# Kernel tuning notes

Hardware: AMD Instinct MI355X
Metric: run time of the kernel (lower is better)

## Reference

```python
import jax, jax.numpy as jnp
import numpy as np

B, T, C, H = 2, 1024, 768, 12
D = C // H
HID = 4 * C
EPS_YAT = 1e-6
EPS_LN = 1e-6


def yat_dense(x, kernel, bias, alpha):
    # scale = (sqrt(n_out)/log(1+n_out))**alpha
    y = x @ kernel
    dist = (jnp.sum(x * x, axis=-1, keepdims=True)
            + jnp.sum(kernel * kernel, axis=0) - 2.0 * y)
    y = (y * y) / (dist + EPS_YAT)
    if bias is not None:
        y = y + bias
    n = kernel.shape[1]
    scale = (jnp.sqrt(jnp.float32(n)) / jnp.log1p(jnp.float32(n))) ** alpha
    return y * scale


def layernorm(x, scale):
    mu = jnp.mean(x, axis=-1, keepdims=True)
    var = jnp.mean((x - mu) ** 2, axis=-1, keepdims=True)
    return (x - mu) * jax.lax.rsqrt(var + EPS_LN) * scale


def rope_table(seq_len, dim):
    freqs = jnp.exp(jnp.arange(0, dim, 2, dtype=jnp.float32)
                    * (-jnp.log(10000.0) / dim))
    angles = jnp.arange(seq_len, dtype=jnp.float32)[:, None] * freqs[None, :]
    return jnp.concatenate([jnp.cos(angles), jnp.sin(angles)], axis=-1)  # [T, D]


def block_forward(x, mask, p):
    Bc, Tc, Cc = x.shape
    h = layernorm(x, p['ln1_scale'])
    qkv = yat_dense(h, p['w_qkv'], p['b_qkv'], p['a_qkv'])  # [B,T,3C]
    qkv = qkv.reshape(Bc, Tc, 3, H, D)
    q, k, v = qkv[:, :, 0], qkv[:, :, 1], qkv[:, :, 2]      # [B,T,H,D]
    rope = rope_table(Tc, D)[:, None, :]                     # [T,1,D]
    q = q * rope
    k = k * rope
    scale = 1.0 / jnp.sqrt(jnp.float32(D))
    attn = jnp.einsum('bihd,bjhd->bhij', q, k) * scale       # [B,H,T,T]
    attn = jnp.where(mask, attn, jnp.finfo(attn.dtype).min)
    attn = jax.nn.softmax(attn, axis=-1)
    o = jnp.einsum('bhij,bjhd->bihd', attn, v).reshape(Bc, Tc, Cc)
    o = yat_dense(o, p['w_ao'], p['b_ao'], p['a_ao'])
    x = x + o
    h = layernorm(x, p['ln2_scale'])
    gate = yat_dense(h, p['w_fc'], p['b_fc'], p['a_fc'])
    u = yat_dense(h, p['w_gate'], p['b_gate'], p['a_gate'])
    u = jax.nn.gelu(u) * gate
    u = yat_dense(u, p['w_proj'], p['b_proj'], p['a_proj'])
    return x + u


def setup_inputs() -> dict:
    key = jax.random.key(0)
    ks = jax.random.split(key, 8)
    x = jax.random.normal(ks[0], (B, T, C), dtype=jnp.float32)
    mask = jnp.tril(jnp.ones((T, T), dtype=bool))[None, None]  # causal [1,1,T,T]
    w = lambda k, shp: 0.02 * jax.random.normal(k, shp, dtype=jnp.float32)
    return {
        'x': x, 'mask': mask,
        'ln1_scale': jnp.ones((C,), jnp.float32),
        'w_qkv': w(ks[1], (C, 3 * C)), 'b_qkv': jnp.zeros((3 * C,), jnp.float32),
        'a_qkv': jnp.ones((1,), jnp.float32),
        'w_ao': w(ks[2], (C, C)), 'b_ao': jnp.zeros((C,), jnp.float32),
        'a_ao': jnp.ones((1,), jnp.float32),
        'ln2_scale': jnp.ones((C,), jnp.float32),
        'w_fc': w(ks[3], (C, HID)), 'b_fc': jnp.zeros((HID,), jnp.float32),
        'a_fc': jnp.ones((1,), jnp.float32),
        'w_gate': w(ks[4], (C, HID)), 'b_gate': jnp.zeros((HID,), jnp.float32),
        'a_gate': jnp.ones((1,), jnp.float32),
        'w_proj': w(ks[5], (HID, C)), 'b_proj': jnp.zeros((C,), jnp.float32),
        'a_proj': jnp.ones((1,), jnp.float32),
    }


def reference(x, mask, ln1_scale, w_qkv, b_qkv, a_qkv, w_ao, b_ao, a_ao,
              ln2_scale, w_fc, b_fc, a_fc, w_gate, b_gate, a_gate,
              w_proj, b_proj, a_proj):
    p = dict(ln1_scale=ln1_scale, w_qkv=w_qkv, b_qkv=b_qkv, a_qkv=a_qkv,
             w_ao=w_ao, b_ao=b_ao, a_ao=a_ao, ln2_scale=ln2_scale,
             w_fc=w_fc, b_fc=b_fc, a_fc=a_fc, w_gate=w_gate, b_gate=b_gate,
             a_gate=a_gate, w_proj=w_proj, b_proj=b_proj, a_proj=a_proj)
    return block_forward(x, mask, p)
```

## Files before the change

kernel.cpp:

```cpp
#include <hip/hip_runtime.h>
#include <cstdint>

#define DEVFN static __device__ __forceinline__

typedef __bf16 bf16x8 __attribute__((ext_vector_type(8)));
typedef float f32x4 __attribute__((ext_vector_type(4)));
typedef unsigned short us4 __attribute__((ext_vector_type(4)));

DEVFN unsigned short f2bf(float f) {
  unsigned u = __float_as_uint(f);
  u += 0x7fffu + ((u >> 16) & 1u);
  return (unsigned short)(u >> 16);
}
DEVFN float bf2f(unsigned short h) { return __uint_as_float(((unsigned)h) << 16); }
DEVFN void async16(const void* g, void* l) {
  __builtin_amdgcn_global_load_lds((__attribute__((address_space(1))) const void*)g,
                                   (__attribute__((address_space(3))) void*)l, 16, 0, 0);
}
DEVFN float gelu_t(float u) {
  return 0.5f * u * (1.f + tanhf(0.7978845608028654f * (u + 0.044715f * u * u * u)));
}
DEVFN int xcd_swizzle(int lin, int total) {
  return (lin & 7) * (total >> 3) + (lin >> 3);
}

struct PrepArgs {
  float* rope;
  const float* W[5]; unsigned short* Wt[5]; float* cn[5];
  int N[5]; int off[6];
  const float* x; const float* g1s; unsigned short* h1; float* hrow1;
};
__global__ __launch_bounds__(256) void k_prep(PrepArgs a) {
  __shared__ float tile[32][33];
  __shared__ float part[8][32];
  __shared__ float red[12];
  const int bid = blockIdx.x, tid = threadIdx.x;
  if (bid < 256) {
    int g = bid * 256 + tid;
    int t = g >> 6, dd = g & 63, i = dd & 31;
    float fr = __expf(-0.2878231366242558f * (float)i);
    float ang = (float)t * fr;
    a.rope[g] = (dd < 32) ? cosf(ang) : sinf(ang);
  } else if (bid < 9472) {
    int lin = bid - 256;
    int e = 0;
    while (lin >= a.off[e + 1]) ++e;
    int local = lin - a.off[e];
    const int N = a.N[e];
    int nbx = N >> 5;
    int tn = local % nbx, tk = local / nbx;
    const float* W = a.W[e];
    unsigned short* Wt = a.Wt[e];
    float* cn = a.cn[e];
    const int K = (e == 4) ? 3072 : 768;
    int tx = tid & 31, ty = tid >> 5;
    float acc = 0.f;
    #pragma unroll
    for (int j = 0; j < 4; ++j) {
      int r = ty + j * 8;
      float v = W[(long)(tk * 32 + r) * N + tn * 32 + tx];
      tile[r][tx] = v;
      acc += v * v;
    }
    part[ty][tx] = acc;
    __syncthreads();
    #pragma unroll
    for (int j = 0; j < 4; ++j) {
      int rr = ty + j * 8;
      Wt[(long)(tn * 32 + rr) * K + tk * 32 + tx] = f2bf(tile[tx][rr]);
    }
    if (ty == 0) {
      float s = part[0][tx];
      #pragma unroll
      for (int jj = 1; jj < 8; ++jj) s += part[jj][tx];
      atomicAdd(&cn[tn * 32 + tx], s);
    }
  } else {
    int row = bid - 9472;
    const float* xr = a.x + (long)row * 768;
    float v0 = xr[tid], v1 = xr[tid + 256], v2 = xr[tid + 512];
    float s = v0 + v1 + v2;
    float ss = v0 * v0 + v1 * v1 + v2 * v2;
    #pragma unroll
    for (int o = 32; o; o >>= 1) { s += __shfl_xor(s, o); ss += __shfl_xor(ss, o); }
    int wv = tid >> 6;
    if ((tid & 63) == 0) { red[wv] = s; red[wv + 4] = ss; }
    __syncthreads();
    s = red[0] + red[1] + red[2] + red[3];
    ss = red[4] + red[5] + red[6] + red[7];
    float mu = s * (1.f / 768.f);
    float var = ss * (1.f / 768.f) - mu * mu;
    float rs = rsqrtf(var + 1e-6f);
    float h0 = (v0 - mu) * rs * a.g1s[tid];
    float h1 = (v1 - mu) * rs * a.g1s[tid + 256];
    float h2 = (v2 - mu) * rs * a.g1s[tid + 512];
    unsigned short* hr = a.h1 + (long)row * 768;
    hr[tid] = f2bf(h0); hr[tid + 256] = f2bf(h1); hr[tid + 512] = f2bf(h2);
    float p = h0 * h0 + h1 * h1 + h2 * h2;
    #pragma unroll
    for (int o = 32; o; o >>= 1) p += __shfl_xor(p, o);
    if ((tid & 63) == 0) red[8 + wv] = p;
    __syncthreads();
    if (tid == 0) a.hrow1[row] = red[8] + red[9] + red[10] + red[11];
  }
}

__global__ __launch_bounds__(256) void k_ln(const float* __restrict__ x,
    const float* __restrict__ g, unsigned short* __restrict__ h, float* __restrict__ row2) {
  int row = blockIdx.x, tid = threadIdx.x;
  const float* xr = x + (long)row * 768;
  float v0 = xr[tid], v1 = xr[tid + 256], v2 = xr[tid + 512];
  float s = v0 + v1 + v2;
  float ss = v0 * v0 + v1 * v1 + v2 * v2;
  #pragma unroll
  for (int o = 32; o; o >>= 1) { s += __shfl_xor(s, o); ss += __shfl_xor(ss, o); }
  __shared__ float red[12];
  int wv = tid >> 6;
  if ((tid & 63) == 0) { red[wv] = s; red[wv + 4] = ss; }
  __syncthreads();
  s = red[0] + red[1] + red[2] + red[3];
  ss = red[4] + red[5] + red[6] + red[7];
  float mu = s * (1.f / 768.f);
  float var = ss * (1.f / 768.f) - mu * mu;
  float rs = rsqrtf(var + 1e-6f);
  float h0 = (v0 - mu) * rs * g[tid];
  float h1 = (v1 - mu) * rs * g[tid + 256];
  float h2 = (v2 - mu) * rs * g[tid + 512];
  unsigned short* hr = h + (long)row * 768;
  hr[tid] = f2bf(h0); hr[tid + 256] = f2bf(h1); hr[tid + 512] = f2bf(h2);
  float p = h0 * h0 + h1 * h1 + h2 * h2;
  #pragma unroll
  for (int o = 32; o; o >>= 1) p += __shfl_xor(p, o);
  if ((tid & 63) == 0) red[8 + wv] = p;
  __syncthreads();
  if (tid == 0) row2[row] = red[8] + red[9] + red[10] + red[11];
}

constexpr int M_QKV = 0, M_AO = 1, M_PART = 2;

struct GemmArgs {
  const unsigned short* A; const unsigned short* Bt;
  const float* arow2; const float* wcol2; const float* bias; const float* alpha;
  int N; int ks;
  const float* rope;
  unsigned short* qo; unsigned short* ko; unsigned short* vo;
  const float* xf; float* xo;
  float* part;
};

template <int MODE, int NI, int NBM, int NBN, int NZ>
__global__ __launch_bounds__(256, 4) void k_gemm(GemmArgs p) {
  __shared__ __align__(16) unsigned short As[3][2048];
  __shared__ __align__(16) unsigned short Bs[3][4096];
  const int tid = threadIdx.x, wave = tid >> 6, lane = tid & 63;
  const int quad = lane >> 4, l = lane & 15;
  constexpr int TOTAL = NBM * NBN * NZ;
  const int g = xcd_swizzle(blockIdx.x, TOTAL);
  const int bm = (g % NBM) * 64;
  const int rest = g / NBM;
  const int bn = (rest % NBN) * 128;
  const int z = rest / NBN;
  const int kb = z * (NI * 32);
  const int ks = p.ks;
  const int wm = (wave & 1) * 32, wn = (wave >> 1) * 64;
  const f32x4 fzero = {0.f, 0.f, 0.f, 0.f};
  f32x4 acc[2][4];
  #pragma unroll
  for (int i = 0; i < 2; ++i)
    #pragma unroll
    for (int j = 0; j < 4; ++j) acc[i][j] = fzero;
  const int sw = (l >> 1) & 3;

  auto stage = [&](int s, int k0) {
    {
      int ci = tid;
      int r = ci >> 2;
      int c = (ci & 3) ^ ((r >> 1) & 3);
      async16(p.A + (long)(bm + r) * ks + kb + k0 + c * 8, &As[s][ci * 8]);
    }
    #pragma unroll
    for (int it = 0; it < 2; ++it) {
      int ci = tid + it * 256;
      int r = ci >> 2;
      int c = (ci & 3) ^ ((r >> 1) & 3);
      async16(p.Bt + (long)(bn + r) * ks + kb + k0 + c * 8, &Bs[s][ci * 8]);
    }
  };
  auto compute = [&](int s) {
    bf16x8 af[2], bfv[4];
    #pragma unroll
    for (int mi = 0; mi < 2; ++mi)
      af[mi] = *(const bf16x8*)&As[s][(wm + mi * 16 + l) * 32 + ((quad ^ sw) * 8)];
    #pragma unroll
    for (int ni = 0; ni < 4; ++ni)
      bfv[ni] = *(const bf16x8*)&Bs[s][(wn + ni * 16 + l) * 32 + ((quad ^ sw) * 8)];
    #pragma unroll
    for (int mi = 0; mi < 2; ++mi)
      #pragma unroll
      for (int ni = 0; ni < 4; ++ni)
        acc[mi][ni] = __builtin_amdgcn_mfma_f32_16x16x32_bf16(af[mi], bfv[ni], acc[mi][ni], 0, 0, 0);
  };
  auto iter = [&](int s, int i) {
    if (i + 1 >= NI) { asm volatile("s_waitcnt vmcnt(0)" ::: "memory"); }
    else             { asm volatile("s_waitcnt vmcnt(3)" ::: "memory"); }
    __builtin_amdgcn_s_barrier();
    asm volatile("" ::: "memory");
    if (i + 2 < NI) stage(s == 0 ? 2 : s - 1, (i + 2) * 32);
    compute(s);
  };

  stage(0, 0);
  stage(1, 32);
  int i = 0;
  while (i < NI) {
    iter(0, i); ++i;
    iter(1, i); ++i;
    iter(2, i); ++i;
  }

  if constexpr (MODE == M_PART) {
    float* slab = p.part + (long)z * (2048 * 768);
    #pragma unroll
    for (int ni = 0; ni < 4; ++ni) {
      const int j = bn + wn + ni * 16 + l;
      #pragma unroll
      for (int mi = 0; mi < 2; ++mi) {
        const int i0 = bm + wm + mi * 16 + quad * 4;
        #pragma unroll
        for (int rg = 0; rg < 4; ++rg)
          slab[(long)(i0 + rg) * 768 + j] = acc[mi][ni][rg];
      }
    }
  } else {
    const float al = p.alpha[0];
    const float nn = (float)p.N;
    const float ys = powf(sqrtf(nn) / log1pf(nn), al);
    #pragma unroll
    for (int ni = 0; ni < 4; ++ni) {
      const int j = bn + wn + ni * 16 + l;
      const float w2 = p.wcol2[j];
      const float bj = p.bias[j];
      int s3 = 0, hh = 0, dd = 0;
      if constexpr (MODE == M_QKV) { s3 = j / 768; int rem = j - s3 * 768; hh = rem >> 6; dd = rem & 63; }
      #pragma unroll
      for (int mi = 0; mi < 2; ++mi) {
        const int i0 = bm + wm + mi * 16 + quad * 4;
        float vv[4];
        #pragma unroll
        for (int rg = 0; rg < 4; ++rg) {
          const float y = acc[mi][ni][rg];
          const float dist = p.arow2[i0 + rg] + w2 - 2.f * y + 1e-6f;
          vv[rg] = (y * y / dist + bj) * ys;
        }
        if constexpr (MODE == M_QKV) {
          int b = i0 >> 10, t0 = i0 & 1023;
          if (s3 == 2) {
            us4 pk = {f2bf(vv[0]), f2bf(vv[1]), f2bf(vv[2]), f2bf(vv[3])};
            *(us4*)&p.vo[((long)(b * 12 + hh) * 64 + dd) * 1024 + t0] = pk;
          } else {
            unsigned short* dst = (s3 == 0) ? p.qo : p.ko;
            #pragma unroll
            for (int rg = 0; rg < 4; ++rg) {
              float ro = p.rope[(t0 + rg) * 64 + dd];
              dst[((long)(b * 12 + hh) * 1024 + t0 + rg) * 64 + dd] = f2bf(vv[rg] * ro);
            }
          }
        } else {
          #pragma unroll
          for (int rg = 0; rg < 4; ++rg) {
            long idx = (long)(i0 + rg) * 768 + j;
            p.xo[idx] = p.xf[idx] + vv[rg];
          }
        }
      }
    }
  }
}

struct EpiArgs {
  const float* slab; const float* arow2; const float* wcol2;
  const float* bias; const float* alpha; const float* xo; float* outf;
};
__global__ __launch_bounds__(256) void k_proj_epi(EpiArgs p) {
  int g = blockIdx.x * 256 + threadIdx.x;
  int i = g / 192, jv = (g - i * 192) * 4;
  long base = (long)i * 768 + jv;
  f32x4 y = *(const f32x4*)(p.slab + base);
  y += *(const f32x4*)(p.slab + 1572864 + base);
  const float a2 = p.arow2[i];
  const float ys = powf(sqrtf(768.f) / log1pf(768.f), p.alpha[0]);
  f32x4 xo4 = *(const f32x4*)(p.xo + base);
  f32x4 out;
  #pragma unroll
  for (int c = 0; c < 4; ++c) {
    float yy = y[c];
    float dist = a2 + p.wcol2[jv + c] - 2.f * yy + 1e-6f;
    out[c] = xo4[c] + (yy * yy / dist + p.bias[jv + c]) * ys;
  }
  *(f32x4*)(p.outf + base) = out;
}

struct MlpArgs {
  const unsigned short* A; const unsigned short* Bf; const unsigned short* Bg;
  const float* arow2; const float* w2f; const float* w2g;
  const float* bf; const float* bg; const float* af_; const float* ag_;
  unsigned short* mlp; float* mrow2;
};

__global__ __launch_bounds__(256, 2) void k_mlp(MlpArgs p) {
  constexpr int NI = 24, K = 768;
  __shared__ __align__(16) unsigned short As[3][4096];
  __shared__ __align__(16) unsigned short Bfs[3][4096];
  __shared__ __align__(16) unsigned short Bgs[3][4096];
  const int tid = threadIdx.x, wave = tid >> 6, lane = tid & 63;
  const int quad = lane >> 4, l = lane & 15;
  const int g = xcd_swizzle(blockIdx.x, 16 * 24);
  const int bm = (g % 16) * 128, bn = (g / 16) * 128;
  const int wm = (wave & 1) * 64, wn = (wave >> 1) * 64;
  const f32x4 fzero = {0.f, 0.f, 0.f, 0.f};
  f32x4 accf[4][4], accg[4][4];
  #pragma unroll
  for (int i = 0; i < 4; ++i)
    #pragma unroll
    for (int j = 0; j < 4; ++j) { accf[i][j] = fzero; accg[i][j] = fzero; }
  const int sw = (l >> 1) & 3;

  auto stage = [&](int s, int k0) {
    #pragma unroll
    for (int it = 0; it < 2; ++it) {
      int ci = tid + it * 256;
      int r = ci >> 2;
      int c = (ci & 3) ^ ((r >> 1) & 3);
      async16(p.A  + (long)(bm + r) * K + k0 + c * 8, &As[s][ci * 8]);
      async16(p.Bf + (long)(bn + r) * K + k0 + c * 8, &Bfs[s][ci * 8]);
      async16(p.Bg + (long)(bn + r) * K + k0 + c * 8, &Bgs[s][ci * 8]);
    }
  };
  auto compute = [&](int s) {
    bf16x8 af[4], bff[4], bfg[4];
    #pragma unroll
    for (int mi = 0; mi < 4; ++mi)
      af[mi] = *(const bf16x8*)&As[s][(wm + mi * 16 + l) * 32 + ((quad ^ sw) * 8)];
    #pragma unroll
    for (int ni = 0; ni < 4; ++ni) {
      bff[ni] = *(const bf16x8*)&Bfs[s][(wn + ni * 16 + l) * 32 + ((quad ^ sw) * 8)];
      bfg[ni] = *(const bf16x8*)&Bgs[s][(wn + ni * 16 + l) * 32 + ((quad ^ sw) * 8)];
    }
    #pragma unroll
    for (int mi = 0; mi < 4; ++mi)
      #pragma unroll
      for (int ni = 0; ni < 4; ++ni) {
        accf[mi][ni] = __builtin_amdgcn_mfma_f32_16x16x32_bf16(af[mi], bff[ni], accf[mi][ni], 0, 0, 0);
        accg[mi][ni] = __builtin_amdgcn_mfma_f32_16x16x32_bf16(af[mi], bfg[ni], accg[mi][ni], 0, 0, 0);
      }
  };
  auto iter = [&](int s, int i) {
    if (i + 1 >= NI) { asm volatile("s_waitcnt vmcnt(0)" ::: "memory"); }
    else             { asm volatile("s_waitcnt vmcnt(6)" ::: "memory"); }
    __builtin_amdgcn_s_barrier();
    asm volatile("" ::: "memory");
    if (i + 2 < NI) stage(s == 0 ? 2 : s - 1, (i + 2) * 32);
    compute(s);
  };

  stage(0, 0);
  stage(1, 32);
  int i = 0;
  while (i < NI) {
    iter(0, i); ++i;
    iter(1, i); ++i;
    iter(2, i); ++i;
  }

  const float ysf = powf(sqrtf(3072.f) / log1pf(3072.f), p.af_[0]);
  const float ysg = powf(sqrtf(3072.f) / log1pf(3072.f), p.ag_[0]);
  float w2f[4], w2g[4], bjf[4], bjg[4]; int js[4];
  #pragma unroll
  for (int ni = 0; ni < 4; ++ni) {
    int j = bn + wn + ni * 16 + l;
    js[ni] = j; w2f[ni] = p.w2f[j]; w2g[ni] = p.w2g[j]; bjf[ni] = p.bf[j]; bjg[ni] = p.bg[j];
  }
  #pragma unroll
  for (int mi = 0; mi < 4; ++mi) {
    #pragma unroll
    for (int rg = 0; rg < 4; ++rg) {
      const int ii = bm + wm + mi * 16 + quad * 4 + rg;
      const float a2 = p.arow2[ii];
      float rsum = 0.f;
      #pragma unroll
      for (int ni = 0; ni < 4; ++ni) {
        float yf = accf[mi][ni][rg];
        float gate = (yf * yf / (a2 + w2f[ni] - 2.f * yf + 1e-6f) + bjf[ni]) * ysf;
        float yg = accg[mi][ni][rg];
        float u  = (yg * yg / (a2 + w2g[ni] - 2.f * yg + 1e-6f) + bjg[ni]) * ysg;
        float out = gelu_t(u) * gate;
        p.mlp[(long)ii * 3072 + js[ni]] = f2bf(out);
        rsum += out * out;
      }
      #pragma unroll
      for (int o = 8; o; o >>= 1) rsum += __shfl_xor(rsum, o);
      if (l == 0) atomicAdd(&p.mrow2[ii], rsum);
    }
  }
}

__global__ __launch_bounds__(256) void k_attn(const unsigned short* __restrict__ qb,
    const unsigned short* __restrict__ kb, const unsigned short* __restrict__ vb,
    unsigned short* __restrict__ ob, float* __restrict__ orow2) {
  __shared__ __align__(16) unsigned short Qs[4096];
  __shared__ __align__(16) unsigned short Ks[3][4096];
  __shared__ __align__(16) unsigned short Vs[3][4096];
  __shared__ __align__(16) unsigned short Ps[4096];
  const int tid = threadIdx.x, wave = tid >> 6, lane = tid & 63;
  const int quad = lane >> 4, l = lane & 15;
  const int g = xcd_swizzle(blockIdx.x, 16 * 24);
  const int bh = g % 24, qt = 15 - (g / 24);
  const int b = bh / 12, hh = bh % 12;
  const int q0 = qt * 64;
  const f32x4 fzero = {0.f, 0.f, 0.f, 0.f};

  auto stage_kv = [&](int s, int jt) {
    const unsigned short* kg = kb + ((long)bh * 1024 + jt * 64) * 64;
    const unsigned short* vg = vb + (long)bh * 64 * 1024 + jt * 64;
    #pragma unroll
    for (int it = 0; it < 2; ++it) {
      int ci = tid + it * 256;
      int r = ci >> 3;
      int c = (ci & 7) ^ (r & 7);
      async16(kg + (long)r * 64 + c * 8, &Ks[s][ci * 8]);
      async16(vg + (long)r * 1024 + c * 8, &Vs[s][ci * 8]);
    }
  };

  const unsigned short* qg = qb + ((long)bh * 1024 + q0) * 64;
  #pragma unroll
  for (int it = 0; it < 2; ++it) {
    int ci = tid + it * 256;
    int r = ci >> 3;
    int c = (ci & 7) ^ (r & 7);
    async16(qg + (long)r * 64 + c * 8, &Qs[ci * 8]);
  }
  stage_kv(0, 0);
  if (qt >= 1) {
    stage_kv(1, 1);
    asm volatile("s_waitcnt vmcnt(4)" ::: "memory");
  } else {
    asm volatile("s_waitcnt vmcnt(0)" ::: "memory");
  }
  __builtin_amdgcn_s_barrier();
  asm volatile("" ::: "memory");

  bf16x8 aq[2];
  #pragma unroll
  for (int ks = 0; ks < 2; ++ks)
    aq[ks] = *(const bf16x8*)&Qs[(wave * 16 + l) * 64 + (((ks * 4 + quad) ^ (l & 7)) * 8)];

  f32x4 O[4];
  float mi_[4], li[4];
  #pragma unroll
  for (int f = 0; f < 4; ++f) O[f] = fzero;
  #pragma unroll
  for (int r = 0; r < 4; ++r) { mi_[r] = -1e30f; li[r] = 0.f; }

  for (int jt = 0; jt <= qt; ++jt) {
    const int s = jt % 3;
    if (jt > 0) {
      if (jt + 1 <= qt) { asm volatile("s_waitcnt vmcnt(4)" ::: "memory"); }
      else              { asm volatile("s_waitcnt vmcnt(0)" ::: "memory"); }
      __builtin_amdgcn_s_barrier();
      asm volatile("" ::: "memory");
    }
    if (jt + 2 <= qt) stage_kv((jt + 2) % 3, jt + 2);

    f32x4 S[4];
    #pragma unroll
    for (int f = 0; f < 4; ++f) S[f] = fzero;
    #pragma unroll
    for (int ks = 0; ks < 2; ++ks) {
      #pragma unroll
      for (int f = 0; f < 4; ++f) {
        bf16x8 bk = *(const bf16x8*)&Ks[s][(f * 16 + l) * 64 + (((ks * 4 + quad) ^ (l & 7)) * 8)];
        S[f] = __builtin_amdgcn_mfma_f32_16x16x32_bf16(aq[ks], bk, S[f], 0, 0, 0);
      }
    }
    const bool diag = (jt == qt);
    #pragma unroll
    for (int f = 0; f < 4; ++f)
      #pragma unroll
      for (int r = 0; r < 4; ++r) {
        float v = S[f][r] * 0.125f;
        if (diag && (f * 16 + l > wave * 16 + quad * 4 + r)) v = -1e30f;
        S[f][r] = v;
      }
    #pragma unroll
    for (int r = 0; r < 4; ++r) {
      float mx = fmaxf(fmaxf(S[0][r], S[1][r]), fmaxf(S[2][r], S[3][r]));
      #pragma unroll
      for (int o = 8; o; o >>= 1) mx = fmaxf(mx, __shfl_xor(mx, o));
      float mnew = fmaxf(mi_[r], mx);
      float alr = __expf(mi_[r] - mnew);
      float sum = 0.f;
      #pragma unroll
      for (int f = 0; f < 4; ++f) {
        float e = __expf(S[f][r] - mnew);
        S[f][r] = e;
        sum += e;
      }
      #pragma unroll
      for (int o = 8; o; o >>= 1) sum += __shfl_xor(sum, o);
      li[r] = li[r] * alr + sum;
      #pragma unroll
      for (int f = 0; f < 4; ++f) O[f][r] *= alr;
      mi_[r] = mnew;
    }
    #pragma unroll
    for (int f = 0; f < 4; ++f)
      #pragma unroll
      for (int r = 0; r < 4; ++r) {
        int i = quad * 4 + r;
        int j = f * 16 + l;
        int pch = (j >> 3) ^ (i & 7);
        Ps[wave * 1024 + i * 64 + pch * 8 + (j & 7)] = f2bf(S[f][r]);
      }
    #pragma unroll
    for (int ks = 0; ks < 2; ++ks) {
      bf16x8 ap = *(const bf16x8*)&Ps[wave * 1024 + l * 64 + (((ks * 4 + quad) ^ (l & 7)) * 8)];
      #pragma unroll
      for (int f = 0; f < 4; ++f) {
        bf16x8 bv = *(const bf16x8*)&Vs[s][(f * 16 + l) * 64 + (((ks * 4 + quad) ^ (l & 7)) * 8)];
        O[f] = __builtin_amdgcn_mfma_f32_16x16x32_bf16(ap, bv, O[f], 0, 0, 0);
      }
    }
  }
  #pragma unroll
  for (int f = 0; f < 4; ++f)
    #pragma unroll
    for (int r = 0; r < 4; ++r) {
      int t = q0 + wave * 16 + quad * 4 + r;
      int dd = f * 16 + l;
      float v = O[f][r] / li[r];
      ob[((long)(b * 1024 + t) * 12 + hh) * 64 + dd] = f2bf(v);
    }
  #pragma unroll
  for (int r = 0; r < 4; ++r) {
    float rsum = 0.f;
    #pragma unroll
    for (int f = 0; f < 4; ++f) { float v = O[f][r] / li[r]; rsum += v * v; }
    #pragma unroll
    for (int o = 8; o; o >>= 1) rsum += __shfl_xor(rsum, o);
    if (l == 0) {
      int t = q0 + wave * 16 + quad * 4 + r;
      atomicAdd(&orow2[b * 1024 + t], rsum);
    }
  }
}

extern "C" void kernel_launch(void* const* d_in, const int* in_sizes, int n_in,
                              void* d_out, int out_size, void* d_ws, size_t ws_size,
                              hipStream_t stream) {
  (void)in_sizes; (void)n_in; (void)out_size;
  char* w = (char*)d_ws;
  size_t off = 0;
  auto alloc = [&](size_t bytes) -> void* {
    void* p = w + off;
    off = (off + bytes + 255) & ~(size_t)255;
    return p;
  };
  float* rope            = (float*)alloc(65536 * 4);
  unsigned short* wtqkv  = (unsigned short*)alloc((size_t)2304 * 768 * 2);
  unsigned short* wtao   = (unsigned short*)alloc((size_t)768 * 768 * 2);
  unsigned short* wtfc   = (unsigned short*)alloc((size_t)3072 * 768 * 2);
  unsigned short* wtgate = (unsigned short*)alloc((size_t)3072 * 768 * 2);
  unsigned short* wtproj = (unsigned short*)alloc((size_t)768 * 3072 * 2);
  float* zeroed          = (float*)alloc(14080 * 4);
  unsigned short* h1     = (unsigned short*)alloc((size_t)2048 * 768 * 2);
  float* hrow1           = (float*)alloc(2048 * 4);
  unsigned short* qbuf   = (unsigned short*)alloc((size_t)2048 * 768 * 2);
  unsigned short* kbuf   = (unsigned short*)alloc((size_t)2048 * 768 * 2);
  unsigned short* vbuf   = (unsigned short*)alloc((size_t)2048 * 768 * 2);
  unsigned short* obuf   = (unsigned short*)alloc((size_t)2048 * 768 * 2);
  float* xo              = (float*)alloc((size_t)2048 * 768 * 4);
  unsigned short* h2     = (unsigned short*)alloc((size_t)2048 * 768 * 2);
  float* hrow2           = (float*)alloc(2048 * 4);
  unsigned short* mlp    = (unsigned short*)alloc((size_t)2048 * 3072 * 2);
  float* slabs           = (float*)alloc((size_t)2 * 2048 * 768 * 4);
  if (off > ws_size) return;

  float* wcol2  = zeroed;
  float* orow2  = zeroed + 9984;
  float* mrow2  = zeroed + 9984 + 2048;
  float* c_qkv  = wcol2 + 0;
  float* c_ao   = wcol2 + 2304;
  float* c_fc   = wcol2 + 3072;
  float* c_gate = wcol2 + 6144;
  float* c_proj = wcol2 + 9216;

  const float* xin = (const float*)d_in[0];

  hipMemsetAsync(zeroed, 0, 14080 * 4, stream);

  PrepArgs pa;
  pa.rope = rope;
  pa.W[0] = (const float*)d_in[3];  pa.Wt[0] = wtqkv;  pa.cn[0] = c_qkv;  pa.N[0] = 2304;
  pa.W[1] = (const float*)d_in[6];  pa.Wt[1] = wtao;   pa.cn[1] = c_ao;   pa.N[1] = 768;
  pa.W[2] = (const float*)d_in[10]; pa.Wt[2] = wtfc;   pa.cn[2] = c_fc;   pa.N[2] = 3072;
  pa.W[3] = (const float*)d_in[13]; pa.Wt[3] = wtgate; pa.cn[3] = c_gate; pa.N[3] = 3072;
  pa.W[4] = (const float*)d_in[16]; pa.Wt[4] = wtproj; pa.cn[4] = c_proj; pa.N[4] = 768;
  pa.off[0] = 0; pa.off[1] = 1728; pa.off[2] = 2304; pa.off[3] = 4608;
  pa.off[4] = 6912; pa.off[5] = 9216;
  pa.x = xin; pa.g1s = (const float*)d_in[2]; pa.h1 = h1; pa.hrow1 = hrow1;
  k_prep<<<11520, 256, 0, stream>>>(pa);

  GemmArgs gq = {};
  gq.A = h1; gq.Bt = wtqkv; gq.arow2 = hrow1; gq.wcol2 = c_qkv;
  gq.bias = (const float*)d_in[4]; gq.alpha = (const float*)d_in[5];
  gq.N = 2304; gq.ks = 768;
  gq.rope = rope; gq.qo = qbuf; gq.ko = kbuf; gq.vo = vbuf;
  k_gemm<M_QKV, 24, 32, 18, 1><<<576, 256, 0, stream>>>(gq);

  k_attn<<<384, 256, 0, stream>>>(qbuf, kbuf, vbuf, obuf, orow2);

  GemmArgs ga = {};
  ga.A = obuf; ga.Bt = wtao; ga.arow2 = orow2; ga.wcol2 = c_ao;
  ga.bias = (const float*)d_in[7]; ga.alpha = (const float*)d_in[8];
  ga.N = 768; ga.ks = 768;
  ga.xf = xin; ga.xo = xo;
  k_gemm<M_AO, 24, 32, 6, 1><<<192, 256, 0, stream>>>(ga);

  k_ln<<<2048, 256, 0, stream>>>(xo, (const float*)d_in[9], h2, hrow2);

  MlpArgs gm = {};
  gm.A = h2; gm.Bf = wtfc; gm.Bg = wtgate; gm.arow2 = hrow2;
  gm.w2f = c_fc; gm.w2g = c_gate;
  gm.bf = (const float*)d_in[11]; gm.bg = (const float*)d_in[14];
  gm.af_ = (const float*)d_in[12]; gm.ag_ = (const float*)d_in[15];
  gm.mlp = mlp; gm.mrow2 = mrow2;
  k_mlp<<<384, 256, 0, stream>>>(gm);

  GemmArgs gp = {};
  gp.A = mlp; gp.Bt = wtproj;
  gp.N = 768; gp.ks = 3072;
  gp.part = slabs;
  k_gemm<M_PART, 48, 32, 6, 2><<<384, 256, 0, stream>>>(gp);

  EpiArgs ge = {};
  ge.slab = slabs; ge.arow2 = mrow2; ge.wcol2 = c_proj;
  ge.bias = (const float*)d_in[17]; ge.alpha = (const float*)d_in[18];
  ge.xo = xo; ge.outf = (float*)d_out;
  k_proj_epi<<<1536, 256, 0, stream>>>(ge);
}
```

Before: 281.1 us.

## Retile MLP GEMM, split-K proj into four bf16 slabs, use fast math

After: 276.7 us. Within noise of the previous version (-1.6%).

```diff
diff --git a/kernel.cpp b/kernel.cpp
--- a/kernel.cpp
+++ b/kernel.cpp
@@ -18,7 +18,10 @@
                                    (__attribute__((address_space(3))) void*)l, 16, 0, 0);
 }
 DEVFN float gelu_t(float u) {
-  return 0.5f * u * (1.f + tanhf(0.7978845608028654f * (u + 0.044715f * u * u * u)));
+  float z = 0.7978845608028654f * (u + 0.044715f * u * u * u);
+  float zc = fminf(fmaxf(z, -15.f), 15.f);
+  float e = __expf(2.f * zc);
+  return u * __fdividef(e, e + 1.f);
 }
 DEVFN int xcd_swizzle(int lin, int total) {
   return (lin & 7) * (total >> 3) + (lin >> 3);
@@ -145,7 +148,7 @@
   const float* rope;
   unsigned short* qo; unsigned short* ko; unsigned short* vo;
   const float* xf; float* xo;
-  float* part;
+  unsigned short* partb;
 };
 
 template <int MODE, int NI, int NBM, int NBN, int NZ>
@@ -219,7 +222,7 @@
   }
 
   if constexpr (MODE == M_PART) {
-    float* slab = p.part + (long)z * (2048 * 768);
+    unsigned short* slab = p.partb + (long)z * (2048 * 768);
     #pragma unroll
     for (int ni = 0; ni < 4; ++ni) {
       const int j = bn + wn + ni * 16 + l;
@@ -228,7 +231,7 @@
         const int i0 = bm + wm + mi * 16 + quad * 4;
         #pragma unroll
         for (int rg = 0; rg < 4; ++rg)
-          slab[(long)(i0 + rg) * 768 + j] = acc[mi][ni][rg];
+          slab[(long)(i0 + rg) * 768 + j] = f2bf(acc[mi][ni][rg]);
       }
     }
   } else {
@@ -250,7 +253,7 @@
         for (int rg = 0; rg < 4; ++rg) {
           const float y = acc[mi][ni][rg];
           const float dist = p.arow2[i0 + rg] + w2 - 2.f * y + 1e-6f;
-          vv[rg] = (y * y / dist + bj) * ys;
+          vv[rg] = (__fdividef(y * y, dist) + bj) * ys;
         }
         if constexpr (MODE == M_QKV) {
           int b = i0 >> 10, t0 = i0 & 1023;
@@ -278,15 +281,20 @@
 }
 
 struct EpiArgs {
-  const float* slab; const float* arow2; const float* wcol2;
+  const unsigned short* slab; const float* arow2; const float* wcol2;
   const float* bias; const float* alpha; const float* xo; float* outf;
 };
 __global__ __launch_bounds__(256) void k_proj_epi(EpiArgs p) {
   int g = blockIdx.x * 256 + threadIdx.x;
   int i = g / 192, jv = (g - i * 192) * 4;
   long base = (long)i * 768 + jv;
-  f32x4 y = *(const f32x4*)(p.slab + base);
-  y += *(const f32x4*)(p.slab + 1572864 + base);
+  f32x4 y = {0.f, 0.f, 0.f, 0.f};
+  #pragma unroll
+  for (int z = 0; z < 4; ++z) {
+    us4 s4 = *(const us4*)(p.slab + (long)z * 1572864 + base);
+    #pragma unroll
+    for (int c = 0; c < 4; ++c) y[c] += bf2f(s4[c]);
+  }
   const float a2 = p.arow2[i];
   const float ys = powf(sqrtf(768.f) / log1pf(768.f), p.alpha[0]);
   f32x4 xo4 = *(const f32x4*)(p.xo + base);
@@ -295,7 +303,7 @@
   for (int c = 0; c < 4; ++c) {
     float yy = y[c];
     float dist = a2 + p.wcol2[jv + c] - 2.f * yy + 1e-6f;
-    out[c] = xo4[c] + (yy * yy / dist + p.bias[jv + c]) * ys;
+    out[c] = xo4[c] + (__fdividef(yy * yy, dist) + p.bias[jv + c]) * ys;
   }
   *(f32x4*)(p.outf + base) = out;
 }
@@ -307,69 +315,61 @@
   unsigned short* mlp; float* mrow2;
 };
 
-__global__ __launch_bounds__(256, 2) void k_mlp(MlpArgs p) {
+__global__ __launch_bounds__(256, 3) void k_mlp(MlpArgs p) {
   constexpr int NI = 24, K = 768;
-  __shared__ __align__(16) unsigned short As[3][4096];
   __shared__ __align__(16) unsigned short Bfs[3][4096];
   __shared__ __align__(16) unsigned short Bgs[3][4096];
   const int tid = threadIdx.x, wave = tid >> 6, lane = tid & 63;
   const int quad = lane >> 4, l = lane & 15;
-  const int g = xcd_swizzle(blockIdx.x, 16 * 24);
-  const int bm = (g % 16) * 128, bn = (g / 16) * 128;
-  const int wm = (wave & 1) * 64, wn = (wave >> 1) * 64;
+  const int g = xcd_swizzle(blockIdx.x, 32 * 24);
+  const int bm = (g % 32) * 64, bn = (g / 32) * 128;
+  const int wm = (wave & 1) * 32, wn = (wave >> 1) * 64;
   const f32x4 fzero = {0.f, 0.f, 0.f, 0.f};
-  f32x4 accf[4][4], accg[4][4];
-  #pragma unroll
-  for (int i = 0; i < 4; ++i)
+  f32x4 accf[2][4], accg[2][4];
+  #pragma unroll
+  for (int i = 0; i < 2; ++i)
     #pragma unroll
     for (int j = 0; j < 4; ++j) { accf[i][j] = fzero; accg[i][j] = fzero; }
   const int sw = (l >> 1) & 3;
 
-  auto stage = [&](int s, int k0) {
+  auto stageB = [&](int s, int k0) {
     #pragma unroll
     for (int it = 0; it < 2; ++it) {
       int ci = tid + it * 256;
       int r = ci >> 2;
       int c = (ci & 3) ^ ((r >> 1) & 3);
-      async16(p.A  + (long)(bm + r) * K + k0 + c * 8, &As[s][ci * 8]);
       async16(p.Bf + (long)(bn + r) * K + k0 + c * 8, &Bfs[s][ci * 8]);
       async16(p.Bg + (long)(bn + r) * K + k0 + c * 8, &Bgs[s][ci * 8]);
     }
   };
-  auto compute = [&](int s) {
-    bf16x8 af[4], bff[4], bfg[4];
-    #pragma unroll
-    for (int mi = 0; mi < 4; ++mi)
-      af[mi] = *(const bf16x8*)&As[s][(wm + mi * 16 + l) * 32 + ((quad ^ sw) * 8)];
+
+  stageB(0, 0);
+  stageB(1, 32);
+  const unsigned short* Arow0 = p.A + (long)(bm + wm + l) * K + quad * 8;
+  const unsigned short* Arow1 = Arow0 + 16 * K;
+  for (int i = 0; i < NI; ++i) {
+    const int s = i % 3;
+    const int k0 = i * 32;
+    bf16x8 af0 = *(const bf16x8*)(Arow0 + k0);
+    bf16x8 af1 = *(const bf16x8*)(Arow1 + k0);
+    if (i + 1 >= NI) { asm volatile("s_waitcnt vmcnt(2)" ::: "memory"); }
+    else             { asm volatile("s_waitcnt vmcnt(6)" ::: "memory"); }
+    __builtin_amdgcn_s_barrier();
+    asm volatile("" ::: "memory");
+    if (i + 2 < NI) stageB((i + 2) % 3, (i + 2) * 32);
+    bf16x8 bff[4], bfg[4];
     #pragma unroll
     for (int ni = 0; ni < 4; ++ni) {
       bff[ni] = *(const bf16x8*)&Bfs[s][(wn + ni * 16 + l) * 32 + ((quad ^ sw) * 8)];
       bfg[ni] = *(const bf16x8*)&Bgs[s][(wn + ni * 16 + l) * 32 + ((quad ^ sw) * 8)];
     }
     #pragma unroll
-    for (int mi = 0; mi < 4; ++mi)
-      #pragma unroll
-      for (int ni = 0; ni < 4; ++ni) {
-        accf[mi][ni] = __builtin_amdgcn_mfma_f32_16x16x32_bf16(af[mi], bff[ni], accf[mi][ni], 0, 0, 0);
-        accg[mi][ni] = __builtin_amdgcn_mfma_f32_16x16x32_bf16(af[mi], bfg[ni], accg[mi][ni], 0, 0, 0);
-      }
-  };
-  auto iter = [&](int s, int i) {
-    if (i + 1 >= NI) { asm volatile("s_waitcnt vmcnt(0)" ::: "memory"); }
-    else             { asm volatile("s_waitcnt vmcnt(6)" ::: "memory"); }
-    __builtin_amdgcn_s_barrier();
-    asm volatile("" ::: "memory");
-    if (i + 2 < NI) stage(s == 0 ? 2 : s - 1, (i + 2) * 32);
-    compute(s);
-  };
-
-  stage(0, 0);
-  stage(1, 32);
-  int i = 0;
-  while (i < NI) {
-    iter(0, i); ++i;
-    iter(1, i); ++i;
-    iter(2, i); ++i;
+    for (int ni = 0; ni < 4; ++ni) {
+      accf[0][ni] = __builtin_amdgcn_mfma_f32_16x16x32_bf16(af0, bff[ni], accf[0][ni], 0, 0, 0);
+      accg[0][ni] = __builtin_amdgcn_mfma_f32_16x16x32_bf16(af0, bfg[ni], accg[0][ni], 0, 0, 0);
+      accf[1][ni] = __builtin_amdgcn_mfma_f32_16x16x32_bf16(af1, bff[ni], accf[1][ni], 0, 0, 0);
+      accg[1][ni] = __builtin_amdgcn_mfma_f32_16x16x32_bf16(af1, bfg[ni], accg[1][ni], 0, 0, 0);
+    }
   }
 
   const float ysf = powf(sqrtf(3072.f) / log1pf(3072.f), p.af_[0]);
@@ -381,7 +381,7 @@
     js[ni] = j; w2f[ni] = p.w2f[j]; w2g[ni] = p.w2g[j]; bjf[ni] = p.bf[j]; bjg[ni] = p.bg[j];
   }
   #pragma unroll
-  for (int mi = 0; mi < 4; ++mi) {
+  for (int mi = 0; mi < 2; ++mi) {
     #pragma unroll
     for (int rg = 0; rg < 4; ++rg) {
       const int ii = bm + wm + mi * 16 + quad * 4 + rg;
@@ -390,9 +390,9 @@
       #pragma unroll
       for (int ni = 0; ni < 4; ++ni) {
         float yf = accf[mi][ni][rg];
-        float gate = (yf * yf / (a2 + w2f[ni] - 2.f * yf + 1e-6f) + bjf[ni]) * ysf;
+        float gate = (__fdividef(yf * yf, a2 + w2f[ni] - 2.f * yf + 1e-6f) + bjf[ni]) * ysf;
         float yg = accg[mi][ni][rg];
-        float u  = (yg * yg / (a2 + w2g[ni] - 2.f * yg + 1e-6f) + bjg[ni]) * ysg;
+        float u  = (__fdividef(yg * yg, a2 + w2g[ni] - 2.f * yg + 1e-6f) + bjg[ni]) * ysg;
         float out = gelu_t(u) * gate;
         p.mlp[(long)ii * 3072 + js[ni]] = f2bf(out);
         rsum += out * out;
@@ -532,20 +532,22 @@
       }
     }
   }
+  float inv[4];
+  #pragma unroll
+  for (int r = 0; r < 4; ++r) inv[r] = __fdividef(1.f, li[r]);
   #pragma unroll
   for (int f = 0; f < 4; ++f)
     #pragma unroll
     for (int r = 0; r < 4; ++r) {
       int t = q0 + wave * 16 + quad * 4 + r;
       int dd = f * 16 + l;
-      float v = O[f][r] / li[r];
-      ob[((long)(b * 1024 + t) * 12 + hh) * 64 + dd] = f2bf(v);
+      ob[((long)(b * 1024 + t) * 12 + hh) * 64 + dd] = f2bf(O[f][r] * inv[r]);
     }
   #pragma unroll
   for (int r = 0; r < 4; ++r) {
     float rsum = 0.f;
     #pragma unroll
-    for (int f = 0; f < 4; ++f) { float v = O[f][r] / li[r]; rsum += v * v; }
+    for (int f = 0; f < 4; ++f) { float v = O[f][r] * inv[r]; rsum += v * v; }
     #pragma unroll
     for (int o = 8; o; o >>= 1) rsum += __shfl_xor(rsum, o);
     if (l == 0) {
@@ -583,7 +585,7 @@
   unsigned short* h2     = (unsigned short*)alloc((size_t)2048 * 768 * 2);
   float* hrow2           = (float*)alloc(2048 * 4);
   unsigned short* mlp    = (unsigned short*)alloc((size_t)2048 * 3072 * 2);
-  float* slabs           = (float*)alloc((size_t)2 * 2048 * 768 * 4);
+  unsigned short* slabs  = (unsigned short*)alloc((size_t)4 * 2048 * 768 * 2);
   if (off > ws_size) return;
 
   float* wcol2  = zeroed;
@@ -635,13 +637,13 @@
   gm.bf = (const float*)d_in[11]; gm.bg = (const float*)d_in[14];
   gm.af_ = (const float*)d_in[12]; gm.ag_ = (const float*)d_in[15];
   gm.mlp = mlp; gm.mrow2 = mrow2;
-  k_mlp<<<384, 256, 0, stream>>>(gm);
+  k_mlp<<<768, 256, 0, stream>>>(gm);
 
   GemmArgs gp = {};
   gp.A = mlp; gp.Bt = wtproj;
   gp.N = 768; gp.ks = 3072;
-  gp.part = slabs;
-  k_gemm<M_PART, 48, 32, 6, 2><<<384, 256, 0, stream>>>(gp);
+  gp.partb = slabs;
+  k_gemm<M_PART, 24, 32, 6, 4><<<768, 256, 0, stream>>>(gp);
 
   EpiArgs ge = {};
   ge.slab = slabs; ge.arow2 = mrow2; ge.wcol2 = c_proj;
```
